# Kernel optimization log

Hardware: AMD Instinct MI355X
Metric: run time of the kernel (lower is better)

The kernel has to match this reference:

```python
import jax, jax.numpy as jnp
import numpy as np

N_NODES = 50000
N_EDGES = 800000
HIDDEN = 128
OUT_DIM = 64


def setup_inputs() -> dict:
    key = jax.random.key(0)
    ks = jax.random.split(key, 8)
    s = 1.0 / np.sqrt(HIDDEN)
    return {
        "z": jax.random.normal(ks[0], (N_NODES, HIDDEN), dtype=jnp.float32),
        "W1": jax.random.uniform(ks[1], (HIDDEN, HIDDEN), jnp.float32, -s, s),
        "b1": jax.random.uniform(ks[2], (HIDDEN,), jnp.float32, -s, s),
        "Wg": jax.random.uniform(ks[3], (HIDDEN, HIDDEN), jnp.float32, -s, s),
        "bg": jnp.zeros((HIDDEN,), jnp.float32),
        "W2": jax.random.uniform(ks[4], (HIDDEN, OUT_DIM), jnp.float32, -s, s),
        "b2": jax.random.uniform(ks[5], (OUT_DIM,), jnp.float32, -s, s),
        "edge_index": jax.random.randint(ks[6], (2, N_EDGES), 0, N_NODES, dtype=jnp.int64),
    }


def gcn_conv(x, Wg, bg, edge_index, n_nodes):
    # PyG GCNConv: add self-loops, symmetric deg^{-1/2} normalization,
    # x' = D^-1/2 (A+I) D^-1/2 (x @ Wg) + bg
    loops = jnp.arange(n_nodes, dtype=edge_index.dtype)
    row = jnp.concatenate([edge_index[0], loops])  # source j
    col = jnp.concatenate([edge_index[1], loops])  # target i
    xw = x @ Wg                                    # [N, H]
    deg = jax.ops.segment_sum(jnp.ones_like(col, dtype=xw.dtype), col,
                              num_segments=n_nodes)
    dinv = jnp.where(deg > 0, jax.lax.rsqrt(deg), 0.0)
    norm = dinv[row] * dinv[col]                   # [E+N]
    msg = xw[row] * norm[:, None]                  # gather + scale
    agg = jax.ops.segment_sum(msg, col, num_segments=n_nodes)  # scatter-add
    return agg + bg


def reference(z, W1, b1, Wg, bg, W2, b2, edge_index):
    n_nodes = z.shape[0]
    h = jax.nn.relu(z @ W1 + b1)
    h = jax.nn.relu(gcn_conv(h, Wg, bg, edge_index, n_nodes))
    out = h @ W2 + b2
    out = out.at[:, 0].set(jax.nn.sigmoid(out[:, 0]))
    return out
```

## Files before the change

### kernel.cpp

```cpp
#include <hip/hip_runtime.h>
#include <hip/hip_bf16.h>
#include <math.h>

#define HID 128
#define ODIM 64
#define NSLICE 8
#define CAP 64

typedef __bf16 bf16x8 __attribute__((ext_vector_type(8)));
typedef float f32x4 __attribute__((ext_vector_type(4)));

union FragU {
  unsigned u[4];
  bf16x8 v;
};

__device__ inline unsigned pack_bf16(float a, float b) {
  unsigned ua = __float_as_uint(a), ub = __float_as_uint(b);
  ua += 0x7fffu + ((ua >> 16) & 1u);
  ub += 0x7fffu + ((ub >> 16) & 1u);
  return (ua >> 16) | (ub & 0xffff0000u);
}
__device__ inline float bf16_lo(unsigned u) { return __uint_as_float(u << 16); }
__device__ inline float bf16_hi(unsigned u) {
  return __uint_as_float(u & 0xffff0000u);
}
__device__ inline unsigned short bf16_of(float v) {
  unsigned uv = __float_as_uint(v);
  uv += 0x7fffu + ((uv >> 16) & 1u);
  return (unsigned short)(uv >> 16);
}

__device__ inline int edge_val(const void* ei, int is64, long long idx) {
  if (is64) return (int)((const long long*)ei)[idx];
  return ((const int*)ei)[idx];
}

__global__ __launch_bounds__(256) void setup_kernel(
    const void* __restrict__ ei, int E, unsigned* __restrict__ rows32,
    unsigned* __restrict__ cols32, const float* __restrict__ W1,
    const float* __restrict__ Wg, const float* __restrict__ W2,
    unsigned* __restrict__ w1h, unsigned* __restrict__ w1l,
    unsigned* __restrict__ wgh, unsigned* __restrict__ wgl,
    unsigned* __restrict__ w2h, unsigned* __restrict__ w2l,
    unsigned* __restrict__ cnt, int n) {
  int bid = blockIdx.x;
  int tid = threadIdx.x;
  if (bid < 20) {
    int e = bid * 256 + tid;
    const float* W;
    unsigned *Wh, *Wl;
    int NC, eo;
    if (e < 2048) {
      W = W1; Wh = w1h; Wl = w1l; NC = 128; eo = e;
    } else if (e < 4096) {
      W = Wg; Wh = wgh; Wl = wgl; NC = 128; eo = e - 2048;
    } else if (e < 5120) {
      W = W2; Wh = w2h; Wl = w2l; NC = 64; eo = e - 4096;
    } else {
      return;
    }
    int lane = eo & 63;
    int s = (eo >> 6) & 3;
    int t = eo >> 8;
    int g = lane >> 4, c = lane & 15;
    int col = t * 16 + c;
    unsigned hw[4], lw[4];
#pragma unroll
    for (int j = 0; j < 4; ++j) {
      float a = W[(32 * s + g * 8 + 2 * j) * NC + col];
      float b = W[(32 * s + g * 8 + 2 * j + 1) * NC + col];
      unsigned h = pack_bf16(a, b);
      hw[j] = h;
      lw[j] = pack_bf16(a - bf16_lo(h), b - bf16_hi(h));
    }
    *(uint4*)&Wh[(size_t)eo * 4] = make_uint4(hw[0], hw[1], hw[2], hw[3]);
    *(uint4*)&Wl[(size_t)eo * 4] = make_uint4(lw[0], lw[1], lw[2], lw[3]);
  } else if (bid < 532) {
    const unsigned* w = (const unsigned*)ei;
    int lane = tid & 63;
    unsigned hv = w[2 * lane + 1];
    int is64 = (__ballot(hv == 0u) == 0xFFFFFFFFFFFFFFFFull) ? 1 : 0;
    int npair = (E + 1) >> 1;
    for (int j = (bid - 20) * 256 + tid; j < npair; j += 512 * 256) {
      int e0 = 2 * j, e1 = 2 * j + 1;
      unsigned r0 = (unsigned)edge_val(ei, is64, e0) & 0xFFFFu;
      unsigned c0 = (unsigned)edge_val(ei, is64, (long long)E + e0) & 0xFFFFu;
      unsigned r1 = 0, c1 = 0;
      if (e1 < E) {
        r1 = (unsigned)edge_val(ei, is64, e1) & 0xFFFFu;
        c1 = (unsigned)edge_val(ei, is64, (long long)E + e1) & 0xFFFFu;
      }
      rows32[j] = r0 | (r1 << 16);
      cols32[j] = c0 | (c1 << 16);
    }
  } else {
    int base = (bid - 532) * 1024 + tid * 4;
    if (base + 4 <= n) {
      *(uint4*)&cnt[base] = make_uint4(0, 0, 0, 0);
    } else {
      for (int j = 0; j < 4; ++j)
        if (base + j < n) cnt[base + j] = 0u;
    }
  }
}

__global__ __launch_bounds__(256) void fill64_kernel(
    const unsigned* __restrict__ rows32, const unsigned* __restrict__ cols32,
    int E, unsigned* __restrict__ cnt, unsigned short* __restrict__ ebuf64,
    int slice_w) {
  int slice = blockIdx.x & (NSLICE - 1);
  int cid = blockIdx.x >> 3;
  int nch = gridDim.x >> 3;
  int lo = slice * slice_w, hi = lo + slice_w;
  int npair = (E + 1) >> 1;
  for (int j = cid * 256 + threadIdx.x; j < npair; j += nch * 256) {
    unsigned rr = rows32[j];
    unsigned cc = cols32[j];
    int c0 = (int)(cc & 0xFFFFu), c1 = (int)(cc >> 16);
    if (c0 >= lo && c0 < hi) {
      unsigned p = atomicAdd(&cnt[c0], 1u);
      if (p < CAP) ebuf64[(size_t)c0 * CAP + p] = (unsigned short)(rr & 0xFFFFu);
    }
    if (2 * j + 1 < E && c1 >= lo && c1 < hi) {
      unsigned p = atomicAdd(&cnt[c1], 1u);
      if (p < CAP) ebuf64[(size_t)c1 * CAP + p] = (unsigned short)(rr >> 16);
    }
  }
}

__global__ __launch_bounds__(256, 4) void gemm1_kernel(
    const float* __restrict__ A, const unsigned* __restrict__ Whi,
    const unsigned* __restrict__ Wlo, const float* __restrict__ bias,
    unsigned short* __restrict__ out, int M) {
  int wave = threadIdx.x >> 6, lane = threadIdx.x & 63;
  int g = lane >> 4, c = lane & 15;
  int tiles_m = (M + 63) >> 6;
  int tiles_total = tiles_m * 2;
  for (int tid = blockIdx.x; tid < tiles_total; tid += gridDim.x) {
    int mt = tid % tiles_m;
    int half = tid / tiles_m;
    int r0 = mt * 64 + wave * 16;
    int rowc = min(r0 + c, M - 1);
    const float* ap = A + (size_t)rowc * 128 + g * 8;
    f32x4 fa[8];
#pragma unroll
    for (int s = 0; s < 4; ++s) {
      fa[2 * s] = *(const f32x4*)(ap + 32 * s);
      fa[2 * s + 1] = *(const f32x4*)(ap + 32 * s + 4);
    }
    f32x4 acc[4];
#pragma unroll
    for (int t = 0; t < 4; ++t) acc[t] = (f32x4){0.f, 0.f, 0.f, 0.f};
#pragma unroll
    for (int s = 0; s < 4; ++s) {
      FragU ah, al;
#pragma unroll
      for (int j = 0; j < 2; ++j) {
        f32x4 p = fa[2 * s + j];
        unsigned h0 = pack_bf16(p[0], p[1]);
        unsigned h1 = pack_bf16(p[2], p[3]);
        ah.u[2 * j] = h0;
        ah.u[2 * j + 1] = h1;
        al.u[2 * j] = pack_bf16(p[0] - bf16_lo(h0), p[1] - bf16_hi(h0));
        al.u[2 * j + 1] = pack_bf16(p[2] - bf16_lo(h1), p[3] - bf16_hi(h1));
      }
#pragma unroll
      for (int tl = 0; tl < 4; ++tl) {
        int e = ((half * 4 + tl) * 4 + s) * 64 + lane;
        FragU wh, wl;
        *(uint4*)wh.u = *(const uint4*)&Whi[(size_t)e * 4];
        *(uint4*)wl.u = *(const uint4*)&Wlo[(size_t)e * 4];
        acc[tl] = __builtin_amdgcn_mfma_f32_16x16x32_bf16(ah.v, wh.v, acc[tl],
                                                          0, 0, 0);
        acc[tl] = __builtin_amdgcn_mfma_f32_16x16x32_bf16(ah.v, wl.v, acc[tl],
                                                          0, 0, 0);
        acc[tl] = __builtin_amdgcn_mfma_f32_16x16x32_bf16(al.v, wh.v, acc[tl],
                                                          0, 0, 0);
      }
    }
#pragma unroll
    for (int tl = 0; tl < 4; ++tl) {
      int colg = half * 64 + tl * 16 + c;
      float bv = bias[colg];
#pragma unroll
      for (int rg = 0; rg < 4; ++rg) {
        int r = r0 + g * 4 + rg;
        if (r < M)
          out[(size_t)r * 128 + colg] = bf16_of(fmaxf(acc[tl][rg] + bv, 0.f));
      }
    }
  }
}

__global__ __launch_bounds__(256, 4) void gemm2_kernel(
    const unsigned short* __restrict__ h16, const unsigned* __restrict__ Whi,
    const unsigned* __restrict__ Wlo, const unsigned* __restrict__ cnt,
    unsigned short* __restrict__ xwbT, int M) {
  int wave = threadIdx.x >> 6, lane = threadIdx.x & 63;
  int g = lane >> 4, c = lane & 15;
  int tiles_m = (M + 63) >> 6;
  int tiles_total = tiles_m * 2;
  for (int tid = blockIdx.x; tid < tiles_total; tid += gridDim.x) {
    int mt = tid % tiles_m;
    int half = tid / tiles_m;
    int r0 = mt * 64 + wave * 16;
    int rowc = min(r0 + c, M - 1);
    const unsigned short* ap = h16 + (size_t)rowc * 128 + g * 8;
    FragU ah[4];
#pragma unroll
    for (int s = 0; s < 4; ++s) *(uint4*)ah[s].u = *(const uint4*)(ap + 32 * s);
    f32x4 acc[4];
#pragma unroll
    for (int t = 0; t < 4; ++t) acc[t] = (f32x4){0.f, 0.f, 0.f, 0.f};
#pragma unroll
    for (int s = 0; s < 4; ++s) {
#pragma unroll
      for (int tl = 0; tl < 4; ++tl) {
        int e = ((half * 4 + tl) * 4 + s) * 64 + lane;
        FragU wh, wl;
        *(uint4*)wh.u = *(const uint4*)&Whi[(size_t)e * 4];
        *(uint4*)wl.u = *(const uint4*)&Wlo[(size_t)e * 4];
        acc[tl] = __builtin_amdgcn_mfma_f32_16x16x32_bf16(ah[s].v, wh.v,
                                                          acc[tl], 0, 0, 0);
        acc[tl] = __builtin_amdgcn_mfma_f32_16x16x32_bf16(ah[s].v, wl.v,
                                                          acc[tl], 0, 0, 0);
      }
    }
    float rs[4];
#pragma unroll
    for (int rg = 0; rg < 4; ++rg) {
      unsigned cv = cnt[min(r0 + g * 4 + rg, M - 1)];
      rs[rg] = rsqrtf((float)(1u + cv));
    }
#pragma unroll
    for (int tl = 0; tl < 4; ++tl) {
      int colg = half * 64 + tl * 16 + c;
      size_t sbase = (size_t)(colg >> 4) * (size_t)M * 16;
      int cw = colg & 15;
#pragma unroll
      for (int rg = 0; rg < 4; ++rg) {
        int r = r0 + g * 4 + rg;
        if (r < M)
          xwbT[sbase + (size_t)r * 16 + cw] = bf16_of(acc[tl][rg] * rs[rg]);
      }
    }
  }
}

__global__ __launch_bounds__(256) void agg_sliced_kernel(
    const unsigned* __restrict__ xwbT, const unsigned* __restrict__ cnt,
    const unsigned short* __restrict__ ebuf64, const float* __restrict__ bg,
    unsigned* __restrict__ h2bT, int n) {
  int slice = blockIdx.x & (NSLICE - 1);
  int lane = threadIdx.x & 63;
  int wave = threadIdx.x >> 6;
  int grp = lane >> 3, lp = lane & 7;
  const unsigned* xs = xwbT + (size_t)slice * n * 8;
  unsigned* hs = h2bT + (size_t)slice * n * 8;
  float2 bgv = ((const float2*)bg)[slice * 8 + lp];
  int wid = (blockIdx.x >> 3) * 4 + wave;
  int nwv = (gridDim.x >> 3) * 4;
  for (int base = wid * 8; base < n; base += nwv * 8) {
    int i = base + grp;
    int act = (i < n);
    int ii = act ? i : 0;
    unsigned cv = cnt[ii];
    int deg = (int)min(cv, (unsigned)CAP);
    float di = rsqrtf((float)(1u + cv));
    unsigned uself = xs[(size_t)ii * 8 + lp];
    float ax = bf16_lo(uself), ay = bf16_hi(uself);
    const unsigned short* el = ebuf64 + (size_t)ii * CAP;
    int t = 0;
    for (; t + 4 <= deg; t += 4) {
      int r0 = el[t], r1 = el[t + 1], r2 = el[t + 2], r3 = el[t + 3];
      unsigned u0 = xs[(size_t)r0 * 8 + lp];
      unsigned u1 = xs[(size_t)r1 * 8 + lp];
      unsigned u2 = xs[(size_t)r2 * 8 + lp];
      unsigned u3 = xs[(size_t)r3 * 8 + lp];
      ax += bf16_lo(u0) + bf16_lo(u1) + bf16_lo(u2) + bf16_lo(u3);
      ay += bf16_hi(u0) + bf16_hi(u1) + bf16_hi(u2) + bf16_hi(u3);
    }
    for (; t < deg; ++t) {
      int r = el[t];
      unsigned u = xs[(size_t)r * 8 + lp];
      ax += bf16_lo(u);
      ay += bf16_hi(u);
    }
    float ox = fmaxf(fmaf(ax, di, bgv.x), 0.f);
    float oy = fmaxf(fmaf(ay, di, bgv.y), 0.f);
    if (act) hs[(size_t)i * 8 + lp] = pack_bf16(ox, oy);
  }
}

__global__ __launch_bounds__(256, 4) void gemmout_kernel(
    const unsigned short* __restrict__ h2bT, const unsigned* __restrict__ Whi,
    const unsigned* __restrict__ Wlo, const float* __restrict__ bias,
    float* __restrict__ out, int M) {
  int wave = threadIdx.x >> 6, lane = threadIdx.x & 63;
  int g = lane >> 4, c = lane & 15;
  int tiles_m = (M + 63) >> 6;
  for (int mt = blockIdx.x; mt < tiles_m; mt += gridDim.x) {
    int r0 = mt * 64 + wave * 16;
    int rowc = min(r0 + c, M - 1);
    FragU ah[4];
#pragma unroll
    for (int s = 0; s < 4; ++s) {
      int k0 = 32 * s + g * 8;
      const unsigned short* ap =
          h2bT + (size_t)(k0 >> 4) * (size_t)M * 16 + (size_t)rowc * 16 +
          (k0 & 15);
      *(uint4*)ah[s].u = *(const uint4*)ap;
    }
    f32x4 acc[4];
#pragma unroll
    for (int t = 0; t < 4; ++t) acc[t] = (f32x4){0.f, 0.f, 0.f, 0.f};
#pragma unroll
    for (int s = 0; s < 4; ++s) {
#pragma unroll
      for (int tl = 0; tl < 4; ++tl) {
        int e = (tl * 4 + s) * 64 + lane;
        FragU wh, wl;
        *(uint4*)wh.u = *(const uint4*)&Whi[(size_t)e * 4];
        *(uint4*)wl.u = *(const uint4*)&Wlo[(size_t)e * 4];
        acc[tl] = __builtin_amdgcn_mfma_f32_16x16x32_bf16(ah[s].v, wh.v,
                                                          acc[tl], 0, 0, 0);
        acc[tl] = __builtin_amdgcn_mfma_f32_16x16x32_bf16(ah[s].v, wl.v,
                                                          acc[tl], 0, 0, 0);
      }
    }
#pragma unroll
    for (int tl = 0; tl < 4; ++tl) {
      int colg = tl * 16 + c;
      float bv = bias[colg];
#pragma unroll
      for (int rg = 0; rg < 4; ++rg) {
        int r = r0 + g * 4 + rg;
        if (r < M) {
          float v = acc[tl][rg] + bv;
          if (colg == 0) v = 1.f / (1.f + __expf(-v));
          out[(size_t)r * ODIM + colg] = v;
        }
      }
    }
  }
}

static inline size_t align16(size_t x) { return (x + 15) & ~(size_t)15; }

extern "C" void kernel_launch(void* const* d_in, const int* in_sizes, int n_in,
                              void* d_out, int out_size, void* d_ws,
                              size_t ws_size, hipStream_t stream) {
  const float* z = (const float*)d_in[0];
  const float* W1 = (const float*)d_in[1];
  const float* b1 = (const float*)d_in[2];
  const float* Wg = (const float*)d_in[3];
  const float* bg = (const float*)d_in[4];
  const float* W2 = (const float*)d_in[5];
  const float* b2 = (const float*)d_in[6];
  const void* ei = d_in[7];

  int N = in_sizes[0] / HID;
  int E = in_sizes[7] / 2;
  int NB = (N + 1023) / 1024;
  int TM = (N + 63) / 64;
  int SLICE_W = (N + NSLICE - 1) / NSLICE;
  int NPAIR = (E + 1) / 2;

  char* ws = (char*)d_ws;
  size_t szB = align16((size_t)N * HID * sizeof(unsigned short));
  unsigned short* h16 = (unsigned short*)ws;
  unsigned* xwbT = (unsigned*)(ws + szB);
  unsigned* h2bT = (unsigned*)(ws + 2 * szB);
  char* p = ws + 3 * szB;
  unsigned int* cnt = (unsigned int*)p;      p += align16((size_t)N * 4);
  unsigned* rows32 = (unsigned*)p;           p += align16((size_t)NPAIR * 4);
  unsigned* cols32 = (unsigned*)p;           p += align16((size_t)NPAIR * 4);
  unsigned short* ebuf64 = (unsigned short*)p;
  p += align16((size_t)N * CAP * 2);
  unsigned* w1h = (unsigned*)p;              p += 2048 * 16;
  unsigned* w1l = (unsigned*)p;              p += 2048 * 16;
  unsigned* wgh = (unsigned*)p;              p += 2048 * 16;
  unsigned* wgl = (unsigned*)p;              p += 2048 * 16;
  unsigned* w2h = (unsigned*)p;              p += 1024 * 16;
  unsigned* w2l = (unsigned*)p;

  setup_kernel<<<532 + NB, 256, 0, stream>>>(ei, E, rows32, cols32, W1, Wg, W2,
                                             w1h, w1l, wgh, wgl, w2h, w2l,
                                             cnt, N);

  gemm1_kernel<<<2 * TM, 256, 0, stream>>>(z, w1h, w1l, b1, h16, N);

  fill64_kernel<<<2048, 256, 0, stream>>>(rows32, cols32, E, cnt, ebuf64,
                                          SLICE_W);

  gemm2_kernel<<<2 * TM, 256, 0, stream>>>(h16, wgh, wgl, cnt,
                                           (unsigned short*)xwbT, N);

  agg_sliced_kernel<<<2048, 256, 0, stream>>>(xwbT, cnt, ebuf64, bg, h2bT, N);

  gemmout_kernel<<<TM, 256, 0, stream>>>((const unsigned short*)h2bT, w2h, w2l,
                                         b2, (float*)d_out, N);
}
```

Before: 147.7 us.

## Bin nodes by degree and vectorize neighbor index loads in aggregation

Adds two small kernels that bucket nodes into eight degree classes and build a permutation, so each aggregation wave processes nodes of similar degree and lane divergence drops. The aggregation loop also loads eight neighbor indices at once with a 16-byte load and guards each gather by a predicate. In exchange it adds two kernel launches, extra atomics and an indirect order lookup, and the output writes become scattered.

```diff
diff --git a/kernel.cpp b/kernel.cpp
--- a/kernel.cpp
+++ b/kernel.cpp
@@ -43,7 +43,7 @@
     unsigned* __restrict__ w1h, unsigned* __restrict__ w1l,
     unsigned* __restrict__ wgh, unsigned* __restrict__ wgl,
     unsigned* __restrict__ w2h, unsigned* __restrict__ w2l,
-    unsigned* __restrict__ cnt, int n) {
+    unsigned* __restrict__ cnt, int nz) {
   int bid = blockIdx.x;
   int tid = threadIdx.x;
   if (bid < 20) {
@@ -96,11 +96,11 @@
     }
   } else {
     int base = (bid - 532) * 1024 + tid * 4;
-    if (base + 4 <= n) {
+    if (base + 4 <= nz) {
       *(uint4*)&cnt[base] = make_uint4(0, 0, 0, 0);
     } else {
       for (int j = 0; j < 4; ++j)
-        if (base + j < n) cnt[base + j] = 0u;
+        if (base + j < nz) cnt[base + j] = 0u;
     }
   }
 }
@@ -129,6 +129,50 @@
   }
 }
 
+__global__ __launch_bounds__(256) void bin_count_kernel(
+    const unsigned* __restrict__ cnt, unsigned* __restrict__ ccnt, int n) {
+  __shared__ unsigned h[8];
+  if (threadIdx.x < 8) h[threadIdx.x] = 0;
+  __syncthreads();
+  for (int i = blockIdx.x * 256 + threadIdx.x; i < n; i += gridDim.x * 256)
+    atomicAdd(&h[min(cnt[i] >> 2, 7u)], 1u);
+  __syncthreads();
+  if (threadIdx.x < 8 && h[threadIdx.x])
+    atomicAdd(&ccnt[threadIdx.x], h[threadIdx.x]);
+}
+
+__global__ __launch_bounds__(256) void bin_scatter_kernel(
+    const unsigned* __restrict__ cnt, const unsigned* __restrict__ ccnt,
+    unsigned* __restrict__ cur, unsigned* __restrict__ order, int n) {
+  __shared__ unsigned h[8];
+  __shared__ unsigned lc[8];
+  int tid = threadIdx.x;
+  if (tid < 8) h[tid] = 0;
+  __syncthreads();
+  int b0 = blockIdx.x * 1024;
+  unsigned cls[4];
+#pragma unroll
+  for (int j = 0; j < 4; ++j) {
+    int i = b0 + j * 256 + tid;
+    cls[j] = (i < n) ? min(cnt[i] >> 2, 7u) : 0xFFu;
+    if (cls[j] != 0xFFu) atomicAdd(&h[cls[j]], 1u);
+  }
+  __syncthreads();
+  if (tid < 8) {
+    unsigned base = 0;
+    for (int k = 0; k < tid; ++k) base += ccnt[k];
+    lc[tid] = base + atomicAdd(&cur[tid], h[tid]);
+  }
+  __syncthreads();
+#pragma unroll
+  for (int j = 0; j < 4; ++j) {
+    if (cls[j] != 0xFFu) {
+      unsigned p = atomicAdd(&lc[cls[j]], 1u);
+      order[p] = (unsigned)(b0 + j * 256 + tid);
+    }
+  }
+}
+
 __global__ __launch_bounds__(256, 4) void gemm1_kernel(
     const float* __restrict__ A, const unsigned* __restrict__ Whi,
     const unsigned* __restrict__ Wlo, const float* __restrict__ bias,
@@ -250,7 +294,8 @@
 
 __global__ __launch_bounds__(256) void agg_sliced_kernel(
     const unsigned* __restrict__ xwbT, const unsigned* __restrict__ cnt,
-    const unsigned short* __restrict__ ebuf64, const float* __restrict__ bg,
+    const unsigned short* __restrict__ ebuf64,
+    const unsigned* __restrict__ order, const float* __restrict__ bg,
     unsigned* __restrict__ h2bT, int n) {
   int slice = blockIdx.x & (NSLICE - 1);
   int lane = threadIdx.x & 63;
@@ -262,30 +307,27 @@
   int wid = (blockIdx.x >> 3) * 4 + wave;
   int nwv = (gridDim.x >> 3) * 4;
   for (int base = wid * 8; base < n; base += nwv * 8) {
-    int i = base + grp;
-    int act = (i < n);
-    int ii = act ? i : 0;
-    unsigned cv = cnt[ii];
+    int slot = base + grp;
+    int act = (slot < n);
+    int i = act ? (int)order[slot] : 0;
+    unsigned cv = cnt[i];
     int deg = (int)min(cv, (unsigned)CAP);
     float di = rsqrtf((float)(1u + cv));
-    unsigned uself = xs[(size_t)ii * 8 + lp];
+    unsigned uself = xs[(size_t)i * 8 + lp];
     float ax = bf16_lo(uself), ay = bf16_hi(uself);
-    const unsigned short* el = ebuf64 + (size_t)ii * CAP;
-    int t = 0;
-    for (; t + 4 <= deg; t += 4) {
-      int r0 = el[t], r1 = el[t + 1], r2 = el[t + 2], r3 = el[t + 3];
-      unsigned u0 = xs[(size_t)r0 * 8 + lp];
-      unsigned u1 = xs[(size_t)r1 * 8 + lp];
-      unsigned u2 = xs[(size_t)r2 * 8 + lp];
-      unsigned u3 = xs[(size_t)r3 * 8 + lp];
-      ax += bf16_lo(u0) + bf16_lo(u1) + bf16_lo(u2) + bf16_lo(u3);
-      ay += bf16_hi(u0) + bf16_hi(u1) + bf16_hi(u2) + bf16_hi(u3);
-    }
-    for (; t < deg; ++t) {
-      int r = el[t];
-      unsigned u = xs[(size_t)r * 8 + lp];
-      ax += bf16_lo(u);
-      ay += bf16_hi(u);
+    const unsigned short* el = ebuf64 + (size_t)i * CAP;
+    for (int t = 0; t < deg; t += 8) {
+      uint4 iv = *(const uint4*)(el + t);
+      unsigned iw[4] = {iv.x, iv.y, iv.z, iv.w};
+#pragma unroll
+      for (int j = 0; j < 8; ++j) {
+        int r = (int)((iw[j >> 1] >> ((j & 1) * 16)) & 0xFFFFu);
+        if (t + j < deg) {
+          unsigned u = xs[(size_t)r * 8 + lp];
+          ax += bf16_lo(u);
+          ay += bf16_hi(u);
+        }
+      }
     }
     float ox = fmaxf(fmaf(ax, di, bgv.x), 0.f);
     float oy = fmaxf(fmaf(ay, di, bgv.y), 0.f);
@@ -362,7 +404,7 @@
 
   int N = in_sizes[0] / HID;
   int E = in_sizes[7] / 2;
-  int NB = (N + 1023) / 1024;
+  int NB = (N + 16 + 1023) / 1024;
   int TM = (N + 63) / 64;
   int SLICE_W = (N + NSLICE - 1) / NSLICE;
   int NPAIR = (E + 1) / 2;
@@ -373,7 +415,10 @@
   unsigned* xwbT = (unsigned*)(ws + szB);
   unsigned* h2bT = (unsigned*)(ws + 2 * szB);
   char* p = ws + 3 * szB;
-  unsigned int* cnt = (unsigned int*)p;      p += align16((size_t)N * 4);
+  unsigned int* cnt = (unsigned int*)p;      p += align16((size_t)(N + 16) * 4);
+  unsigned* ccnt = cnt + N;
+  unsigned* cur = cnt + N + 8;
+  unsigned* order = (unsigned*)p;            p += align16((size_t)N * 4);
   unsigned* rows32 = (unsigned*)p;           p += align16((size_t)NPAIR * 4);
   unsigned* cols32 = (unsigned*)p;           p += align16((size_t)NPAIR * 4);
   unsigned short* ebuf64 = (unsigned short*)p;
@@ -387,17 +432,22 @@
 
   setup_kernel<<<532 + NB, 256, 0, stream>>>(ei, E, rows32, cols32, W1, Wg, W2,
                                              w1h, w1l, wgh, wgl, w2h, w2l,
-                                             cnt, N);
+                                             cnt, N + 16);
 
   gemm1_kernel<<<2 * TM, 256, 0, stream>>>(z, w1h, w1l, b1, h16, N);
 
   fill64_kernel<<<2048, 256, 0, stream>>>(rows32, cols32, E, cnt, ebuf64,
                                           SLICE_W);
 
+  bin_count_kernel<<<49, 256, 0, stream>>>(cnt, ccnt, N);
+  bin_scatter_kernel<<<(N + 1023) / 1024, 256, 0, stream>>>(cnt, ccnt, cur,
+                                                            order, N);
+
   gemm2_kernel<<<2 * TM, 256, 0, stream>>>(h16, wgh, wgl, cnt,
                                            (unsigned short*)xwbT, N);
 
-  agg_sliced_kernel<<<2048, 256, 0, stream>>>(xwbT, cnt, ebuf64, bg, h2bT, N);
+  agg_sliced_kernel<<<2048, 256, 0, stream>>>(xwbT, cnt, ebuf64, order, bg,
+                                              h2bT, N);
 
   gemmout_kernel<<<TM, 256, 0, stream>>>((const unsigned short*)h2bT, w2h, w2l,
                                          b2, (float*)d_out, N);
```

After: 160.0 us. +8.3%, slower.

## Switch aggregation to row-major layout with one wave per node

Applied to the files above, without the earlier changes.

Replaces the feature-sliced transposed buffers with row-major bf16 rows. The aggregation kernel now uses one full wave per destination node, and neighbor indices are loaded as wave-uniform scalars via readfirstlane with 8-way unrolling. This gives fully coalesced 256-byte gathers and fewer per-lane index loads. The trade-off is losing the smaller per-slice working set that may have helped cache hit rates, and low-degree nodes leave wave work sparse.

```diff
diff --git a/kernel.cpp b/kernel.cpp
--- a/kernel.cpp
+++ b/kernel.cpp
@@ -196,7 +196,7 @@
 __global__ __launch_bounds__(256, 4) void gemm2_kernel(
     const unsigned short* __restrict__ h16, const unsigned* __restrict__ Whi,
     const unsigned* __restrict__ Wlo, const unsigned* __restrict__ cnt,
-    unsigned short* __restrict__ xwbT, int M) {
+    unsigned short* __restrict__ xwb, int M) {
   int wave = threadIdx.x >> 6, lane = threadIdx.x & 63;
   int g = lane >> 4, c = lane & 15;
   int tiles_m = (M + 63) >> 6;
@@ -236,65 +236,80 @@
 #pragma unroll
     for (int tl = 0; tl < 4; ++tl) {
       int colg = half * 64 + tl * 16 + c;
-      size_t sbase = (size_t)(colg >> 4) * (size_t)M * 16;
-      int cw = colg & 15;
 #pragma unroll
       for (int rg = 0; rg < 4; ++rg) {
         int r = r0 + g * 4 + rg;
         if (r < M)
-          xwbT[sbase + (size_t)r * 16 + cw] = bf16_of(acc[tl][rg] * rs[rg]);
-      }
-    }
-  }
-}
-
-__global__ __launch_bounds__(256) void agg_sliced_kernel(
-    const unsigned* __restrict__ xwbT, const unsigned* __restrict__ cnt,
+          xwb[(size_t)r * 128 + colg] = bf16_of(acc[tl][rg] * rs[rg]);
+      }
+    }
+  }
+}
+
+__global__ __launch_bounds__(256) void agg_kernel(
+    const unsigned* __restrict__ xwb, const unsigned* __restrict__ cnt,
     const unsigned short* __restrict__ ebuf64, const float* __restrict__ bg,
-    unsigned* __restrict__ h2bT, int n) {
-  int slice = blockIdx.x & (NSLICE - 1);
+    unsigned* __restrict__ h2b, int n) {
   int lane = threadIdx.x & 63;
-  int wave = threadIdx.x >> 6;
-  int grp = lane >> 3, lp = lane & 7;
-  const unsigned* xs = xwbT + (size_t)slice * n * 8;
-  unsigned* hs = h2bT + (size_t)slice * n * 8;
-  float2 bgv = ((const float2*)bg)[slice * 8 + lp];
-  int wid = (blockIdx.x >> 3) * 4 + wave;
-  int nwv = (gridDim.x >> 3) * 4;
-  for (int base = wid * 8; base < n; base += nwv * 8) {
-    int i = base + grp;
-    int act = (i < n);
-    int ii = act ? i : 0;
-    unsigned cv = cnt[ii];
+  int wid = (blockIdx.x * blockDim.x + threadIdx.x) >> 6;
+  int nw = (gridDim.x * blockDim.x) >> 6;
+  float2 bgv = ((const float2*)bg)[lane];
+  for (int i = wid; i < n; i += nw) {
+    unsigned cv = cnt[i];
     int deg = (int)min(cv, (unsigned)CAP);
     float di = rsqrtf((float)(1u + cv));
-    unsigned uself = xs[(size_t)ii * 8 + lp];
+    unsigned uself = xwb[(size_t)i * 64 + lane];
     float ax = bf16_lo(uself), ay = bf16_hi(uself);
-    const unsigned short* el = ebuf64 + (size_t)ii * CAP;
+    const unsigned short* el = ebuf64 + (size_t)i * CAP;
     int t = 0;
+    for (; t + 8 <= deg; t += 8) {
+      int r0 = __builtin_amdgcn_readfirstlane(el[t]);
+      int r1 = __builtin_amdgcn_readfirstlane(el[t + 1]);
+      int r2 = __builtin_amdgcn_readfirstlane(el[t + 2]);
+      int r3 = __builtin_amdgcn_readfirstlane(el[t + 3]);
+      int r4 = __builtin_amdgcn_readfirstlane(el[t + 4]);
+      int r5 = __builtin_amdgcn_readfirstlane(el[t + 5]);
+      int r6 = __builtin_amdgcn_readfirstlane(el[t + 6]);
+      int r7 = __builtin_amdgcn_readfirstlane(el[t + 7]);
+      unsigned u0 = xwb[(size_t)r0 * 64 + lane];
+      unsigned u1 = xwb[(size_t)r1 * 64 + lane];
+      unsigned u2 = xwb[(size_t)r2 * 64 + lane];
+      unsigned u3 = xwb[(size_t)r3 * 64 + lane];
+      unsigned u4 = xwb[(size_t)r4 * 64 + lane];
+      unsigned u5 = xwb[(size_t)r5 * 64 + lane];
+      unsigned u6 = xwb[(size_t)r6 * 64 + lane];
+      unsigned u7 = xwb[(size_t)r7 * 64 + lane];
+      ax += bf16_lo(u0) + bf16_lo(u1) + bf16_lo(u2) + bf16_lo(u3) +
+            bf16_lo(u4) + bf16_lo(u5) + bf16_lo(u6) + bf16_lo(u7);
+      ay += bf16_hi(u0) + bf16_hi(u1) + bf16_hi(u2) + bf16_hi(u3) +
+            bf16_hi(u4) + bf16_hi(u5) + bf16_hi(u6) + bf16_hi(u7);
+    }
     for (; t + 4 <= deg; t += 4) {
-      int r0 = el[t], r1 = el[t + 1], r2 = el[t + 2], r3 = el[t + 3];
-      unsigned u0 = xs[(size_t)r0 * 8 + lp];
-      unsigned u1 = xs[(size_t)r1 * 8 + lp];
-      unsigned u2 = xs[(size_t)r2 * 8 + lp];
-      unsigned u3 = xs[(size_t)r3 * 8 + lp];
+      int r0 = __builtin_amdgcn_readfirstlane(el[t]);
+      int r1 = __builtin_amdgcn_readfirstlane(el[t + 1]);
+      int r2 = __builtin_amdgcn_readfirstlane(el[t + 2]);
+      int r3 = __builtin_amdgcn_readfirstlane(el[t + 3]);
+      unsigned u0 = xwb[(size_t)r0 * 64 + lane];
+      unsigned u1 = xwb[(size_t)r1 * 64 + lane];
+      unsigned u2 = xwb[(size_t)r2 * 64 + lane];
+      unsigned u3 = xwb[(size_t)r3 * 64 + lane];
       ax += bf16_lo(u0) + bf16_lo(u1) + bf16_lo(u2) + bf16_lo(u3);
       ay += bf16_hi(u0) + bf16_hi(u1) + bf16_hi(u2) + bf16_hi(u3);
     }
     for (; t < deg; ++t) {
-      int r = el[t];
-      unsigned u = xs[(size_t)r * 8 + lp];
+      int r = __builtin_amdgcn_readfirstlane(el[t]);
+      unsigned u = xwb[(size_t)r * 64 + lane];
       ax += bf16_lo(u);
       ay += bf16_hi(u);
     }
     float ox = fmaxf(fmaf(ax, di, bgv.x), 0.f);
     float oy = fmaxf(fmaf(ay, di, bgv.y), 0.f);
-    if (act) hs[(size_t)i * 8 + lp] = pack_bf16(ox, oy);
+    h2b[(size_t)i * 64 + lane] = pack_bf16(ox, oy);
   }
 }
 
 __global__ __launch_bounds__(256, 4) void gemmout_kernel(
-    const unsigned short* __restrict__ h2bT, const unsigned* __restrict__ Whi,
+    const unsigned short* __restrict__ h2b, const unsigned* __restrict__ Whi,
     const unsigned* __restrict__ Wlo, const float* __restrict__ bias,
     float* __restrict__ out, int M) {
   int wave = threadIdx.x >> 6, lane = threadIdx.x & 63;
@@ -303,15 +318,10 @@
   for (int mt = blockIdx.x; mt < tiles_m; mt += gridDim.x) {
     int r0 = mt * 64 + wave * 16;
     int rowc = min(r0 + c, M - 1);
+    const unsigned short* ap = h2b + (size_t)rowc * 128 + g * 8;
     FragU ah[4];
 #pragma unroll
-    for (int s = 0; s < 4; ++s) {
-      int k0 = 32 * s + g * 8;
-      const unsigned short* ap =
-          h2bT + (size_t)(k0 >> 4) * (size_t)M * 16 + (size_t)rowc * 16 +
-          (k0 & 15);
-      *(uint4*)ah[s].u = *(const uint4*)ap;
-    }
+    for (int s = 0; s < 4; ++s) *(uint4*)ah[s].u = *(const uint4*)(ap + 32 * s);
     f32x4 acc[4];
 #pragma unroll
     for (int t = 0; t < 4; ++t) acc[t] = (f32x4){0.f, 0.f, 0.f, 0.f};
@@ -370,8 +380,8 @@
   char* ws = (char*)d_ws;
   size_t szB = align16((size_t)N * HID * sizeof(unsigned short));
   unsigned short* h16 = (unsigned short*)ws;
-  unsigned* xwbT = (unsigned*)(ws + szB);
-  unsigned* h2bT = (unsigned*)(ws + 2 * szB);
+  unsigned* xwb = (unsigned*)(ws + szB);
+  unsigned* h2b = (unsigned*)(ws + 2 * szB);
   char* p = ws + 3 * szB;
   unsigned int* cnt = (unsigned int*)p;      p += align16((size_t)N * 4);
   unsigned* rows32 = (unsigned*)p;           p += align16((size_t)NPAIR * 4);
@@ -395,10 +405,10 @@
                                           SLICE_W);
 
   gemm2_kernel<<<2 * TM, 256, 0, stream>>>(h16, wgh, wgl, cnt,
-                                           (unsigned short*)xwbT, N);
-
-  agg_sliced_kernel<<<2048, 256, 0, stream>>>(xwbT, cnt, ebuf64, bg, h2bT, N);
-
-  gemmout_kernel<<<TM, 256, 0, stream>>>((const unsigned short*)h2bT, w2h, w2l,
+                                           (unsigned short*)xwb, N);
+
+  agg_kernel<<<2048, 256, 0, stream>>>(xwb, cnt, ebuf64, bg, h2b, N);
+
+  gemmout_kernel<<<TM, 256, 0, stream>>>((const unsigned short*)h2b, w2h, w2l,
                                          b2, (float*)d_out, N);
 }
```

Result: faster. 134.6 us, median of 2 (-8.9%).
